# Optimization experiments

Hardware: AMD Instinct MI355X
Metric: run time of the kernel (lower is better)

The kernel has to match this reference:

```python
import jax, jax.numpy as jnp
import numpy as np

B, C, H, W, WS, SH, NH, P = 64, 512, 28, 28, 7, 3, 16, 10
MLP_H = 2048
EPS = 1e-5
NW = (H // WS) * (W // WS)  # 16 windows per image
N = P + WS * WS             # 59 tokens per window
HEAD_D = C // NH
SCALE = HEAD_D ** -0.5


def _rel_pos_index(ws):
    coords = np.stack(np.meshgrid(np.arange(ws), np.arange(ws), indexing='ij')).reshape(2, -1)
    rel = (coords[:, :, None] - coords[:, None, :]).transpose(1, 2, 0)
    rel[..., 0] += ws - 1
    rel[..., 1] += ws - 1
    rel[..., 0] *= 2 * ws - 1
    return rel.sum(-1)  # (ws*ws, ws*ws)


def _attn_mask(h, w, ws, shift):
    img = np.zeros((h, w), dtype=np.float32)
    slices = (slice(0, -ws), slice(-ws, -shift), slice(-shift, None))
    cnt = 0
    for hs in slices:
        for wsl in slices:
            img[hs, wsl] = cnt
            cnt += 1
    mw = img.reshape(h // ws, ws, w // ws, ws).transpose(0, 2, 1, 3).reshape(-1, ws * ws)
    diff = mw[:, None, :] - mw[:, :, None]
    return np.where(diff != 0, -100.0, 0.0).astype(np.float32)  # (nW, ws*ws, ws*ws)


_RPI = jnp.asarray(_rel_pos_index(WS))
_MASK = jnp.asarray(_attn_mask(H, W, WS, SH))


def _ln(x, g, b):
    mu = jnp.mean(x, -1, keepdims=True)
    var = jnp.mean((x - mu) ** 2, -1, keepdims=True)
    return (x - mu) * jax.lax.rsqrt(var + EPS) * g + b


def _window_partition(x, ws):
    b, h, w, c = x.shape
    x = x.reshape(b, h // ws, ws, w // ws, ws, c).transpose(0, 1, 3, 2, 4, 5)
    return x.reshape(-1, ws, ws, c)


def _window_reverse(win, ws, h, w):
    b = win.shape[0] // ((h // ws) * (w // ws))
    x = win.reshape(b, h // ws, w // ws, ws, ws, -1).transpose(0, 1, 3, 2, 4, 5)
    return x.reshape(b, h, w, -1)


def setup_inputs() -> dict:
    key = jax.random.key(0)
    ks = jax.random.split(key, 8)
    d = {
        'x': jax.random.normal(ks[0], (B, P + H * W, C), jnp.float32),
        'g1': jnp.ones((C,), jnp.float32),
        'b1': jnp.zeros((C,), jnp.float32),
        'qkv_w': jax.random.normal(ks[1], (3 * C, C), jnp.float32) * 0.02,
        'qkv_b': jnp.zeros((3 * C,), jnp.float32),
        'rpb_table': jax.random.normal(ks[2], ((2 * WS - 1) ** 2, NH), jnp.float32) * 0.02,
        'proj_w': jax.random.normal(ks[3], (C, C), jnp.float32) * 0.02,
        'proj_b': jnp.zeros((C,), jnp.float32),
        'g2': jnp.ones((C,), jnp.float32),
        'b2': jnp.zeros((C,), jnp.float32),
        'fc1_w': jax.random.normal(ks[4], (MLP_H, C), jnp.float32) * 0.02,
        'fc1_b': jnp.zeros((MLP_H,), jnp.float32),
        'fc2_w': jax.random.normal(ks[5], (C, MLP_H), jnp.float32) * 0.02,
        'fc2_b': jnp.zeros((C,), jnp.float32),
    }
    return d


def _block(x, g1, b1, qkv_w, qkv_b, rpb_table, proj_w, proj_b, g2, b2, fc1_w, fc1_b, fc2_w, fc2_b):
    prompt = x[:, :P, :]                       # (B, P, C)
    x = x[:, P:, :]                            # (B, H*W, C)
    shortcut = x
    xn = _ln(x, g1, b1).reshape(B, H, W, C)
    # cyclic shift
    xn = jnp.roll(xn, shift=(-SH, -SH), axis=(1, 2))
    xw = _window_partition(xn, WS).reshape(-1, WS * WS, C)  # (B*nW, 49, C)
    # prompt padding (matches torch expand(nW,...).reshape order: index = w*B + b)
    pw = jnp.broadcast_to(prompt[None], (NW, B, P, C)).reshape(-1, P, C)
    xw = jnp.concatenate([pw, xw], axis=1)     # (B*nW, N, C)
    B_ = B * NW
    # attention
    qkv = (xw @ qkv_w.T + qkv_b).reshape(B_, N, 3, NH, HEAD_D).transpose(2, 0, 3, 1, 4)
    q, k, v = qkv[0], qkv[1], qkv[2]
    attn = jnp.einsum('bhnd,bhmd->bhnm', q * SCALE, k)  # (B_, NH, N, N)
    bias = rpb_table[_RPI.reshape(-1)].reshape(WS * WS, WS * WS, NH).transpose(2, 0, 1)
    bias = jnp.pad(bias, ((0, 0), (P, 0), (P, 0)))       # (NH, N, N)
    mask = jnp.pad(_MASK, ((0, 0), (P, 0), (P, 0)))      # (nW, N, N)
    attn = attn + bias[None]
    attn = attn.reshape(B, NW, NH, N, N) + mask[None, :, None]
    attn = jax.nn.softmax(attn.reshape(B_, NH, N, N), axis=-1)
    out = jnp.einsum('bhnm,bhmd->bhnd', attn, v).transpose(0, 2, 1, 3).reshape(B_, N, C)
    out = out @ proj_w.T + proj_b
    # drop prompts, un-window, un-shift
    out = out[:, P:, :].reshape(-1, WS, WS, C)
    xs = _window_reverse(out, WS, H, W)
    xs = jnp.roll(xs, shift=(SH, SH), axis=(1, 2)).reshape(B, H * W, C)
    x = shortcut + xs
    # MLP (exact GELU, as torch nn.GELU)
    h = _ln(x, g2, b2)
    h = jax.nn.gelu(h @ fc1_w.T + fc1_b, approximate=False)
    h = h @ fc2_w.T + fc2_b
    return x + h


def reference(x, g1, b1, qkv_w, qkv_b, rpb_table, proj_w, proj_b, g2, b2, fc1_w, fc1_b, fc2_w, fc2_b):
    return _block(x, g1, b1, qkv_w, qkv_b, rpb_table, proj_w, proj_b, g2, b2, fc1_w, fc1_b, fc2_w, fc2_b)
```

## Files before the change

kernel.cpp:

```cpp
#include <hip/hip_runtime.h>
#include <stdint.h>

typedef unsigned short u16;
typedef unsigned int u32;
typedef __attribute__((ext_vector_type(8))) short short8;
typedef __attribute__((ext_vector_type(4))) float f32x4;

__device__ __forceinline__ u16 f2bf(float f) {
  u32 u = __builtin_bit_cast(u32, f);
  u32 r = u + 0x7FFFu + ((u >> 16) & 1u);
  return (u16)(r >> 16);
}

__device__ __forceinline__ void gl_lds16(const void* g, void* l) {
  __builtin_amdgcn_global_load_lds((__attribute__((address_space(1))) void*)g,
                                   (__attribute__((address_space(3))) void*)l,
                                   16, 0, 0);
}

__global__ __launch_bounds__(256) void cvt_bf16(const float* __restrict__ in,
                                                u16* __restrict__ out, int n4) {
  int idx = blockIdx.x * 256 + threadIdx.x;
  if (idx < n4) {
    float4 v = ((const float4*)in)[idx];
    u32 lo = (u32)f2bf(v.x) | ((u32)f2bf(v.y) << 16);
    u32 hi = (u32)f2bf(v.z) | ((u32)f2bf(v.w) << 16);
    ((uint2*)out)[idx] = make_uint2(lo, hi);
  }
}

__global__ __launch_bounds__(256) void ln1_kernel(const float* __restrict__ x,
                                                  const float* __restrict__ g,
                                                  const float* __restrict__ bta,
                                                  u16* __restrict__ xcat) {
  int wave = threadIdx.x >> 6, lane = threadIdx.x & 63;
  int row = blockIdx.x * 4 + wave;
  const float* src;
  bool do_ln;
  if (row < 640) {
    int bb = row / 10, p = row - bb * 10;
    src = x + ((size_t)bb * 794 + p) * 512;
    do_ln = false;
  } else {
    int r2 = row - 640;
    int i = r2 / 49, t = r2 - i * 49;
    int bb = i >> 4, nw = i & 15;
    int tr = t / 7, tc = t - tr * 7;
    int hh = (nw >> 2) * 7 + tr + 3; if (hh >= 28) hh -= 28;
    int ww = (nw & 3) * 7 + tc + 3;  if (ww >= 28) ww -= 28;
    src = x + ((size_t)bb * 794 + 10 + hh * 28 + ww) * 512;
    do_ln = true;
  }
  float4 v0 = ((const float4*)src)[lane * 2];
  float4 v1 = ((const float4*)src)[lane * 2 + 1];
  float vals[8] = {v0.x, v0.y, v0.z, v0.w, v1.x, v1.y, v1.z, v1.w};
  u16 ob[8];
  if (do_ln) {
    float s = 0.f, s2 = 0.f;
#pragma unroll
    for (int j = 0; j < 8; ++j) { s += vals[j]; s2 += vals[j] * vals[j]; }
#pragma unroll
    for (int o = 32; o > 0; o >>= 1) { s += __shfl_xor(s, o); s2 += __shfl_xor(s2, o); }
    float mu = s * (1.0f / 512.0f);
    float var = s2 * (1.0f / 512.0f) - mu * mu;
    float inv = rsqrtf(var + 1e-5f);
    float4 ga = ((const float4*)g)[lane * 2], gb = ((const float4*)g)[lane * 2 + 1];
    float4 ba = ((const float4*)bta)[lane * 2], bb2 = ((const float4*)bta)[lane * 2 + 1];
    float gv[8] = {ga.x, ga.y, ga.z, ga.w, gb.x, gb.y, gb.z, gb.w};
    float bv[8] = {ba.x, ba.y, ba.z, ba.w, bb2.x, bb2.y, bb2.z, bb2.w};
#pragma unroll
    for (int j = 0; j < 8; ++j) ob[j] = f2bf((vals[j] - mu) * inv * gv[j] + bv[j]);
  } else {
#pragma unroll
    for (int j = 0; j < 8; ++j) ob[j] = f2bf(vals[j]);
  }
  u32 w0 = (u32)ob[0] | ((u32)ob[1] << 16);
  u32 w1 = (u32)ob[2] | ((u32)ob[3] << 16);
  u32 w2 = (u32)ob[4] | ((u32)ob[5] << 16);
  u32 w3 = (u32)ob[6] | ((u32)ob[7] << 16);
  ((uint4*)(xcat + (size_t)row * 512))[lane] = make_uint4(w0, w1, w2, w3);
}

__global__ __launch_bounds__(256) void ln2_kernel(const float* __restrict__ xn,
                                                  const float* __restrict__ g,
                                                  const float* __restrict__ bta,
                                                  u16* __restrict__ outb) {
  int wave = threadIdx.x >> 6, lane = threadIdx.x & 63;
  size_t row = (size_t)blockIdx.x * 4 + wave;
  const float* src = xn + row * 512;
  float4 v0 = ((const float4*)src)[lane * 2];
  float4 v1 = ((const float4*)src)[lane * 2 + 1];
  float vals[8] = {v0.x, v0.y, v0.z, v0.w, v1.x, v1.y, v1.z, v1.w};
  float s = 0.f, s2 = 0.f;
#pragma unroll
  for (int j = 0; j < 8; ++j) { s += vals[j]; s2 += vals[j] * vals[j]; }
#pragma unroll
  for (int o = 32; o > 0; o >>= 1) { s += __shfl_xor(s, o); s2 += __shfl_xor(s2, o); }
  float mu = s * (1.0f / 512.0f);
  float var = s2 * (1.0f / 512.0f) - mu * mu;
  float inv = rsqrtf(var + 1e-5f);
  float4 ga = ((const float4*)g)[lane * 2], gb = ((const float4*)g)[lane * 2 + 1];
  float4 ba = ((const float4*)bta)[lane * 2], bb2 = ((const float4*)bta)[lane * 2 + 1];
  float gv[8] = {ga.x, ga.y, ga.z, ga.w, gb.x, gb.y, gb.z, gb.w};
  float bv[8] = {ba.x, ba.y, ba.z, ba.w, bb2.x, bb2.y, bb2.z, bb2.w};
  u16 ob[8];
#pragma unroll
  for (int j = 0; j < 8; ++j) ob[j] = f2bf((vals[j] - mu) * inv * gv[j] + bv[j]);
  u32 w0 = (u32)ob[0] | ((u32)ob[1] << 16);
  u32 w1 = (u32)ob[2] | ((u32)ob[3] << 16);
  u32 w2 = (u32)ob[4] | ((u32)ob[5] << 16);
  u32 w3 = (u32)ob[6] | ((u32)ob[7] << 16);
  ((uint4*)(outb + row * 512))[lane] = make_uint4(w0, w1, w2, w3);
}

template <int EPI>
__global__ __launch_bounds__(512, 2) void gemm256(const u16* __restrict__ A,
                                                  const u16* __restrict__ Wt,
                                                  const float* __restrict__ bias,
                                                  u16* __restrict__ outb,
                                                  float* __restrict__ outf,
                                                  const float* __restrict__ res,
                                                  int M, int N, int K, int Ntiles) {
  __shared__ __align__(16) u16 Al[2][256 * 64];
  __shared__ __align__(16) u16 Bl[2][256 * 64];
  const int tid = threadIdx.x;
  const int lane = tid & 63;
  const int wv = tid >> 6;
  const int wm = wv >> 2, wn = wv & 3;
  const int lr = lane & 15;
  const int qh = lane >> 4;

  const int nwg = gridDim.x;
  const int qx = nwg >> 3, rx = nwg & 7;
  const int xcd = blockIdx.x & 7, local = blockIdx.x >> 3;
  const int swz = (xcd < rx ? xcd * (qx + 1) : rx * (qx + 1) + (xcd - rx) * qx) + local;
  const int mt = swz / Ntiles, nt = swz - mt * Ntiles;
  const int tm = mt * 256, tn = nt * 256;

  f32x4 acc[8][4];
#pragma unroll
  for (int m = 0; m < 8; ++m)
#pragma unroll
    for (int n = 0; n < 4; ++n)
#pragma unroll
      for (int e = 0; e < 4; ++e) acc[m][n][e] = 0.f;

  const int slot = tid & 7;
  const int r0 = tid >> 3;
  const int scol = ((slot ^ (r0 & 7)) << 3);
  const u16* Ap0 = A + (size_t)(tm + r0) * K + scol;
  const u16* Ap1 = A + (size_t)(tm + r0 + 64) * K + scol;
  const u16* Ap2 = A + (size_t)(tm + r0 + 128) * K + scol;
  const u16* Ap3 = A + (size_t)(tm + r0 + 192) * K + scol;
  const u16* Bp0 = Wt + (size_t)(tn + r0) * K + scol;
  const u16* Bp1 = Wt + (size_t)(tn + r0 + 64) * K + scol;
  const u16* Bp2 = Wt + (size_t)(tn + r0 + 128) * K + scol;
  const u16* Bp3 = Wt + (size_t)(tn + r0 + 192) * K + scol;

#define STAGE(buf, k0)                                      \
  do {                                                      \
    u16* al = &Al[buf][tid * 8];                            \
    u16* bl = &Bl[buf][tid * 8];                            \
    gl_lds16(Ap0 + (k0), al);                               \
    gl_lds16(Ap1 + (k0), al + 4096);                        \
    gl_lds16(Ap2 + (k0), al + 8192);                        \
    gl_lds16(Ap3 + (k0), al + 12288);                       \
    gl_lds16(Bp0 + (k0), bl);                               \
    gl_lds16(Bp1 + (k0), bl + 4096);                        \
    gl_lds16(Bp2 + (k0), bl + 8192);                        \
    gl_lds16(Bp3 + (k0), bl + 12288);                       \
  } while (0)

  const int NT = K >> 6;
  STAGE(0, 0);

  for (int t = 0; t < NT; ++t) {
    const int cur = t & 1;
    if (t + 1 < NT) {
      __builtin_amdgcn_s_barrier();
      asm volatile("" ::: "memory");
      STAGE(cur ^ 1, (t + 1) << 6);
      asm volatile("s_waitcnt vmcnt(8)" ::: "memory");
    } else {
      asm volatile("s_waitcnt vmcnt(0)" ::: "memory");
    }
    __builtin_amdgcn_s_barrier();
    asm volatile("" ::: "memory");

    const u16* Ab = &Al[cur][0];
    const u16* Bb = &Bl[cur][0];
#pragma unroll
    for (int ks = 0; ks < 2; ++ks) {
      const int sw = (((ks << 2) | qh) ^ (lr & 7)) << 3;
      short8 av[8], bv[4];
#pragma unroll
      for (int m = 0; m < 8; ++m)
        av[m] = *(const short8*)&Ab[(wm * 128 + m * 16 + lr) * 64 + sw];
#pragma unroll
      for (int n = 0; n < 4; ++n)
        bv[n] = *(const short8*)&Bb[(wn * 64 + n * 16 + lr) * 64 + sw];
      __builtin_amdgcn_s_setprio(1);
#pragma unroll
      for (int m = 0; m < 8; ++m)
#pragma unroll
        for (int n = 0; n < 4; ++n)
          acc[m][n] = __builtin_amdgcn_mfma_f32_16x16x32_bf16(av[m], bv[n], acc[m][n], 0, 0, 0);
      __builtin_amdgcn_s_setprio(0);
    }
    asm volatile("" ::: "memory");
  }
#undef STAGE

  float bcol[4];
#pragma unroll
  for (int n = 0; n < 4; ++n) bcol[n] = bias[tn + wn * 64 + n * 16 + lr];

#pragma unroll
  for (int m = 0; m < 8; ++m) {
#pragma unroll
    for (int r2 = 0; r2 < 4; ++r2) {
      int grow = tm + wm * 128 + m * 16 + qh * 4 + r2;
      if (grow >= M) continue;
      if (EPI == 1) {
        int i = grow / 49, t = grow - i * 49;
        int bb = i >> 4, nw = i & 15;
        int tr = t / 7, tc = t - tr * 7;
        int hh = (nw >> 2) * 7 + tr + 3; if (hh >= 28) hh -= 28;
        int ww = (nw & 3) * 7 + tc + 3;  if (ww >= 28) ww -= 28;
        size_t dstr = ((size_t)bb * 784 + hh * 28 + ww) * 512;
        size_t srcr = ((size_t)bb * 794 + 10 + hh * 28 + ww) * 512;
#pragma unroll
        for (int n = 0; n < 4; ++n) {
          int gcol = tn + wn * 64 + n * 16 + lr;
          float v = acc[m][n][r2] + bcol[n];
          outf[dstr + gcol] = v + res[srcr + gcol];
        }
      } else {
#pragma unroll
        for (int n = 0; n < 4; ++n) {
          int gcol = tn + wn * 64 + n * 16 + lr;
          float v = acc[m][n][r2] + bcol[n];
          if (EPI == 0) {
            outb[(size_t)grow * N + gcol] = f2bf(v);
          } else if (EPI == 2) {
            float gel = 0.5f * v * (1.0f + erff(v * 0.70710678118654752f));
            outb[(size_t)grow * N + gcol] = f2bf(gel);
          } else {
            outf[(size_t)grow * N + gcol] = v + res[(size_t)grow * 512 + gcol];
          }
        }
      }
    }
  }
}

__global__ __launch_bounds__(64) void attn_kernel(const u16* __restrict__ Y,
                                                  const float* __restrict__ rpb,
                                                  u16* __restrict__ outp) {
  __shared__ __align__(16) u16 Plds[64 * 64];
  __shared__ __align__(16) u16 Vt[32 * 64];
  __shared__ float biasl[169];
  const int lane = threadIdx.x;
  const int i = blockIdx.x >> 4;
  const int hd = blockIdx.x & 15;
  const int bp = i & 63;
  const int nw = i & 15;
  const int hi = nw >> 2, wi = nw & 3;
  const int lr = lane & 15;
  const int lk = (lane >> 4) * 8;

  for (int j = lane; j < 169; j += 64) biasl[j] = rpb[j * 16 + hd];

  short8 qf[4], kf[4];
#pragma unroll
  for (int m = 0; m < 4; ++m) {
    int t = m * 16 + lr;
    size_t r = (t < 10) ? (size_t)(bp * 10 + t) : (size_t)(640 + i * 49 + (t - 10));
    const u16* base = Y + r * 1536 + hd * 32 + lk;
    if (t < 59) {
      qf[m] = *(const short8*)(base);
      kf[m] = *(const short8*)(base + 512);
    } else {
#pragma unroll
      for (int e = 0; e < 8; ++e) { qf[m][e] = 0; kf[m][e] = 0; }
    }
  }
  {
    int t = lane;
    if (t < 59) {
      size_t r = (t < 10) ? (size_t)(bp * 10 + t) : (size_t)(640 + i * 49 + (t - 10));
      const u16* vp = Y + r * 1536 + 1024 + hd * 32;
      short8 vv0 = *(const short8*)(vp);
      short8 vv1 = *(const short8*)(vp + 8);
      short8 vv2 = *(const short8*)(vp + 16);
      short8 vv3 = *(const short8*)(vp + 24);
#pragma unroll
      for (int e = 0; e < 8; ++e) {
        Vt[e * 64 + t] = (u16)vv0[e];
        Vt[(8 + e) * 64 + t] = (u16)vv1[e];
        Vt[(16 + e) * 64 + t] = (u16)vv2[e];
        Vt[(24 + e) * 64 + t] = (u16)vv3[e];
      }
    } else {
      for (int d = 0; d < 32; ++d) Vt[d * 64 + t] = 0;
    }
  }

  f32x4 s[4][4];
#pragma unroll
  for (int m = 0; m < 4; ++m)
#pragma unroll
    for (int n = 0; n < 4; ++n)
#pragma unroll
      for (int r2 = 0; r2 < 4; ++r2) s[m][n][r2] = 0.f;
#pragma unroll
  for (int m = 0; m < 4; ++m)
#pragma unroll
    for (int n = 0; n < 4; ++n)
      s[m][n] = __builtin_amdgcn_mfma_f32_16x16x32_bf16(qf[m], kf[n], s[m][n], 0, 0, 0);

  __syncthreads();

  const float SCALE = 0.17677669529663687f;
  const int rgrp = lane >> 4;
#pragma unroll
  for (int m = 0; m < 4; ++m) {
#pragma unroll
    for (int r2 = 0; r2 < 4; ++r2) {
      int rn = m * 16 + rgrp * 4 + r2;
      int qa = rn - 10;
      int qra = qa / 7, qca = qa - qra * 7;
      int regA = 0;
      if (qa >= 0 && qa < 49) {
        int ha = hi * 7 + qra, wa = wi * 7 + qca;
        regA = (ha < 21 ? 0 : (ha < 25 ? 1 : 2)) * 3 + (wa < 21 ? 0 : (wa < 25 ? 1 : 2));
      }
      float vloc[4];
      float mx = -3.0e38f;
#pragma unroll
      for (int n = 0; n < 4; ++n) {
        int cm = n * 16 + lr;
        float v;
        if (cm >= 59) {
          v = -3.0e38f;
        } else {
          v = s[m][n][r2] * SCALE;
          if (rn >= 10 && rn < 59 && cm >= 10) {
            int kb = cm - 10;
            int krb = kb / 7, kcb = kb - krb * 7;
            v += biasl[(qra - krb + 6) * 13 + (qca - kcb + 6)];
            int hb = hi * 7 + krb, wb = wi * 7 + kcb;
            int regB = (hb < 21 ? 0 : (hb < 25 ? 1 : 2)) * 3 + (wb < 21 ? 0 : (wb < 25 ? 1 : 2));
            if (regA != regB) v -= 100.0f;
          }
        }
        vloc[n] = v;
        mx = fmaxf(mx, v);
      }
#pragma unroll
      for (int o = 8; o > 0; o >>= 1) mx = fmaxf(mx, __shfl_xor(mx, o));
      float sum = 0.f;
#pragma unroll
      for (int n = 0; n < 4; ++n) {
        float e = __expf(vloc[n] - mx);
        vloc[n] = e;
        sum += e;
      }
#pragma unroll
      for (int o = 8; o > 0; o >>= 1) sum += __shfl_xor(sum, o);
      float inv = 1.0f / sum;
#pragma unroll
      for (int n = 0; n < 4; ++n)
        Plds[rn * 64 + n * 16 + lr] = f2bf(vloc[n] * inv);
    }
  }

  __syncthreads();

  f32x4 o[4][2];
#pragma unroll
  for (int m = 0; m < 4; ++m)
#pragma unroll
    for (int j = 0; j < 2; ++j)
#pragma unroll
      for (int r2 = 0; r2 < 4; ++r2) o[m][j][r2] = 0.f;
#pragma unroll
  for (int ks = 0; ks < 2; ++ks) {
    short8 pf[4], vf[2];
#pragma unroll
    for (int m = 0; m < 4; ++m)
      pf[m] = *(const short8*)&Plds[(m * 16 + lr) * 64 + ks * 32 + lk];
#pragma unroll
    for (int j = 0; j < 2; ++j)
      vf[j] = *(const short8*)&Vt[(j * 16 + lr) * 64 + ks * 32 + lk];
#pragma unroll
    for (int m = 0; m < 4; ++m)
#pragma unroll
      for (int j = 0; j < 2; ++j)
        o[m][j] = __builtin_amdgcn_mfma_f32_16x16x32_bf16(pf[m], vf[j], o[m][j], 0, 0, 0);
  }

#pragma unroll
  for (int m = 0; m < 4; ++m) {
#pragma unroll
    for (int r2 = 0; r2 < 4; ++r2) {
      int rn = m * 16 + rgrp * 4 + r2;
      if (rn >= 10 && rn < 59) {
        size_t row = (size_t)i * 49 + (rn - 10);
        u16* op = outp + row * 512 + hd * 32;
        op[lr] = f2bf(o[m][0][r2]);
        op[16 + lr] = f2bf(o[m][1][r2]);
      }
    }
  }
}

extern "C" void kernel_launch(void* const* d_in, const int* in_sizes, int n_in,
                              void* d_out, int out_size, void* d_ws, size_t ws_size,
                              hipStream_t stream) {
  const float* x = (const float*)d_in[0];
  const float* g1 = (const float*)d_in[1];
  const float* b1 = (const float*)d_in[2];
  const float* qkv_w = (const float*)d_in[3];
  const float* qkv_b = (const float*)d_in[4];
  const float* rpb = (const float*)d_in[5];
  const float* proj_w = (const float*)d_in[6];
  const float* proj_b = (const float*)d_in[7];
  const float* g2 = (const float*)d_in[8];
  const float* b2 = (const float*)d_in[9];
  const float* fc1_w = (const float*)d_in[10];
  const float* fc1_b = (const float*)d_in[11];
  const float* fc2_w = (const float*)d_in[12];
  const float* fc2_b = (const float*)d_in[13];
  float* out = (float*)d_out;

  char* ws = (char*)d_ws;
  u16* qkv_wb = (u16*)(ws + 0);
  u16* proj_wb = (u16*)(ws + 1572864);
  u16* fc1_wb = (u16*)(ws + 2097152);
  u16* fc2_wb = (u16*)(ws + 4194304);
  u16* xcat = (u16*)(ws + 6291456);
  u16* y = (u16*)(ws + 58327040);
  u16* attnv = (u16*)(ws + 214433792);
  float* xnew = (float*)(ws + 265814016);
  u16* hin = xcat;
  u16* hmid = y;

  cvt_bf16<<<768, 256, 0, stream>>>(qkv_w, qkv_wb, 196608);
  cvt_bf16<<<256, 256, 0, stream>>>(proj_w, proj_wb, 65536);
  cvt_bf16<<<1024, 256, 0, stream>>>(fc1_w, fc1_wb, 262144);
  cvt_bf16<<<1024, 256, 0, stream>>>(fc2_w, fc2_wb, 262144);

  ln1_kernel<<<12704, 256, 0, stream>>>(x, g1, b1, xcat);

  gemm256<0><<<199 * 6, 512, 0, stream>>>(xcat, qkv_wb, qkv_b, y, nullptr, nullptr,
                                          50816, 1536, 512, 6);

  attn_kernel<<<16384, 64, 0, stream>>>(y, rpb, attnv);

  gemm256<1><<<196 * 2, 512, 0, stream>>>(attnv, proj_wb, proj_b, nullptr, xnew, x,
                                          50176, 512, 512, 2);

  ln2_kernel<<<12544, 256, 0, stream>>>(xnew, g2, b2, hin);

  gemm256<2><<<196 * 8, 512, 0, stream>>>(hin, fc1_wb, fc1_b, hmid, nullptr, nullptr,
                                          50176, 2048, 512, 8);

  gemm256<3><<<196 * 2, 512, 0, stream>>>(hmid, fc2_wb, fc2_b, nullptr, out, xnew,
                                          50176, 512, 2048, 2);
}
```

Measured before the change: 821.9 us.

## Restructure GEMM main loop into 4-stage K=32 pipeline with split A/B prefetch

Replaces the double-buffered K=64 LDS staging with a four-buffer ring of K=32 tiles, prefetching three steps ahead. Each iteration is split into two half-N MFMA phases separated by barriers, with A and B loads for a future stage issued between them. The aim is to keep more global loads in flight and interleave memory and MFMA work. In exchange there are more barriers per K step, and the new XOR swizzle and the hand-set vmcnt counts near the loop tail must be exactly right.

```diff
diff --git a/kernel.cpp b/kernel.cpp
--- a/kernel.cpp
+++ b/kernel.cpp
@@ -121,14 +121,15 @@
                                                   float* __restrict__ outf,
                                                   const float* __restrict__ res,
                                                   int M, int N, int K, int Ntiles) {
-  __shared__ __align__(16) u16 Al[2][256 * 64];
-  __shared__ __align__(16) u16 Bl[2][256 * 64];
+  __shared__ __align__(16) u16 Asm[4][256 * 32];
+  __shared__ __align__(16) u16 Bsm[4][256 * 32];
   const int tid = threadIdx.x;
   const int lane = tid & 63;
   const int wv = tid >> 6;
   const int wm = wv >> 2, wn = wv & 3;
   const int lr = lane & 15;
   const int qh = lane >> 4;
+  const int swz8 = (qh ^ ((lr >> 1) & 3)) << 3;
 
   const int nwg = gridDim.x;
   const int qx = nwg >> 3, rx = nwg & 7;
@@ -145,71 +146,87 @@
 #pragma unroll
       for (int e = 0; e < 4; ++e) acc[m][n][e] = 0.f;
 
-  const int slot = tid & 7;
-  const int r0 = tid >> 3;
-  const int scol = ((slot ^ (r0 & 7)) << 3);
-  const u16* Ap0 = A + (size_t)(tm + r0) * K + scol;
-  const u16* Ap1 = A + (size_t)(tm + r0 + 64) * K + scol;
-  const u16* Ap2 = A + (size_t)(tm + r0 + 128) * K + scol;
-  const u16* Ap3 = A + (size_t)(tm + r0 + 192) * K + scol;
-  const u16* Bp0 = Wt + (size_t)(tn + r0) * K + scol;
-  const u16* Bp1 = Wt + (size_t)(tn + r0 + 64) * K + scol;
-  const u16* Bp2 = Wt + (size_t)(tn + r0 + 128) * K + scol;
-  const u16* Bp3 = Wt + (size_t)(tn + r0 + 192) * K + scol;
-
-#define STAGE(buf, k0)                                      \
-  do {                                                      \
-    u16* al = &Al[buf][tid * 8];                            \
-    u16* bl = &Bl[buf][tid * 8];                            \
-    gl_lds16(Ap0 + (k0), al);                               \
-    gl_lds16(Ap1 + (k0), al + 4096);                        \
-    gl_lds16(Ap2 + (k0), al + 8192);                        \
-    gl_lds16(Ap3 + (k0), al + 12288);                       \
-    gl_lds16(Bp0 + (k0), bl);                               \
-    gl_lds16(Bp1 + (k0), bl + 4096);                        \
-    gl_lds16(Bp2 + (k0), bl + 8192);                        \
-    gl_lds16(Bp3 + (k0), bl + 12288);                       \
+  const int sr = tid >> 2;
+  const int sl = tid & 3;
+  const int scol = (sl ^ ((sr >> 1) & 3)) << 3;
+  const u16* Ap0 = A + (size_t)(tm + sr) * K + scol;
+  const u16* Ap1 = A + (size_t)(tm + 128 + sr) * K + scol;
+  const u16* Bp0 = Wt + (size_t)(tn + sr) * K + scol;
+  const u16* Bp1 = Wt + (size_t)(tn + 128 + sr) * K + scol;
+
+#define STAGE_A(buf, k0)                          \
+  do {                                            \
+    u16* d = &Asm[buf][tid * 8];                  \
+    gl_lds16(Ap0 + (k0), d);                      \
+    gl_lds16(Ap1 + (k0), d + 4096);               \
   } while (0)
-
-  const int NT = K >> 6;
-  STAGE(0, 0);
+#define STAGE_B(buf, k0)                          \
+  do {                                            \
+    u16* d = &Bsm[buf][tid * 8];                  \
+    gl_lds16(Bp0 + (k0), d);                      \
+    gl_lds16(Bp1 + (k0), d + 4096);               \
+  } while (0)
+
+  const int NT = K >> 5;
+
+  STAGE_A(0, 0);  STAGE_B(0, 0);
+  STAGE_A(1, 32); STAGE_B(1, 32);
+  STAGE_A(2, 64); STAGE_B(2, 64);
+  asm volatile("s_waitcnt vmcnt(8)" ::: "memory");
+  __builtin_amdgcn_s_barrier();
 
   for (int t = 0; t < NT; ++t) {
-    const int cur = t & 1;
-    if (t + 1 < NT) {
-      __builtin_amdgcn_s_barrier();
-      asm volatile("" ::: "memory");
-      STAGE(cur ^ 1, (t + 1) << 6);
-      asm volatile("s_waitcnt vmcnt(8)" ::: "memory");
-    } else {
-      asm volatile("s_waitcnt vmcnt(0)" ::: "memory");
-    }
+    const int b = t & 3;
+    const u16* Ab = &Asm[b][0];
+    const u16* Bb = &Bsm[b][0];
+    const int pf = t + 3;
+    const int pb = pf & 3;
+    const int pk = pf << 5;
+
+    short8 av[8], bv0[2];
+#pragma unroll
+    for (int m = 0; m < 8; ++m)
+      av[m] = *(const short8*)&Ab[(wm * 128 + m * 16 + lr) * 32 + swz8];
+#pragma unroll
+    for (int n = 0; n < 2; ++n)
+      bv0[n] = *(const short8*)&Bb[(wn * 64 + n * 16 + lr) * 32 + swz8];
+    if (pf < NT) STAGE_A(pb, pk);
+    asm volatile("" ::: "memory");
     __builtin_amdgcn_s_barrier();
+    asm volatile("s_waitcnt lgkmcnt(0)" ::: "memory");
+    __builtin_amdgcn_sched_barrier(0);
+    __builtin_amdgcn_s_setprio(1);
+#pragma unroll
+    for (int m = 0; m < 8; ++m)
+#pragma unroll
+      for (int n = 0; n < 2; ++n)
+        acc[m][n] = __builtin_amdgcn_mfma_f32_16x16x32_bf16(av[m], bv0[n], acc[m][n], 0, 0, 0);
+    __builtin_amdgcn_s_setprio(0);
+    __builtin_amdgcn_s_barrier();
+
+    short8 bv1[2];
+#pragma unroll
+    for (int n = 0; n < 2; ++n)
+      bv1[n] = *(const short8*)&Bb[(wn * 64 + (n + 2) * 16 + lr) * 32 + swz8];
+    if (pf < NT) STAGE_B(pb, pk);
+    if (t <= NT - 4)      asm volatile("s_waitcnt vmcnt(8)" ::: "memory");
+    else if (t == NT - 3) asm volatile("s_waitcnt vmcnt(4)" ::: "memory");
+    else if (t == NT - 2) asm volatile("s_waitcnt vmcnt(0)" ::: "memory");
     asm volatile("" ::: "memory");
-
-    const u16* Ab = &Al[cur][0];
-    const u16* Bb = &Bl[cur][0];
-#pragma unroll
-    for (int ks = 0; ks < 2; ++ks) {
-      const int sw = (((ks << 2) | qh) ^ (lr & 7)) << 3;
-      short8 av[8], bv[4];
-#pragma unroll
-      for (int m = 0; m < 8; ++m)
-        av[m] = *(const short8*)&Ab[(wm * 128 + m * 16 + lr) * 64 + sw];
-#pragma unroll
-      for (int n = 0; n < 4; ++n)
-        bv[n] = *(const short8*)&Bb[(wn * 64 + n * 16 + lr) * 64 + sw];
-      __builtin_amdgcn_s_setprio(1);
-#pragma unroll
-      for (int m = 0; m < 8; ++m)
-#pragma unroll
-        for (int n = 0; n < 4; ++n)
-          acc[m][n] = __builtin_amdgcn_mfma_f32_16x16x32_bf16(av[m], bv[n], acc[m][n], 0, 0, 0);
-      __builtin_amdgcn_s_setprio(0);
-    }
-    asm volatile("" ::: "memory");
-  }
-#undef STAGE
+    __builtin_amdgcn_s_barrier();
+    asm volatile("s_waitcnt lgkmcnt(0)" ::: "memory");
+    __builtin_amdgcn_sched_barrier(0);
+    __builtin_amdgcn_s_setprio(1);
+#pragma unroll
+    for (int m = 0; m < 8; ++m)
+#pragma unroll
+      for (int n = 0; n < 2; ++n)
+        acc[m][n + 2] = __builtin_amdgcn_mfma_f32_16x16x32_bf16(av[m], bv1[n], acc[m][n + 2], 0, 0, 0);
+    __builtin_amdgcn_s_setprio(0);
+    __builtin_amdgcn_s_barrier();
+  }
+#undef STAGE_A
+#undef STAGE_B
 
   float bcol[4];
 #pragma unroll
```

Measured after the change: 802.4 us. 2.4% less time.
